# Optimization experiments

Hardware: AMD Instinct MI355X
Metric: run time of the kernel (lower is better)

Reference implementation:

```python
import jax, jax.numpy as jnp
import numpy as np

B, D, U = 64, 256, 256

def setup_inputs() -> dict:
    key = jax.random.key(0)
    ks = jax.random.split(key, 16)
    init_mu = 0.05
    inputs = jax.random.normal(ks[0], (B, D), jnp.float32)
    prev_state = 0.1 * jax.random.normal(ks[1], (B, U), jnp.float32)
    A = jax.random.normal(ks[2], (B, U, U), jnp.float32)
    # symmetric, diagonally boosted covariance-like state
    Sigma_state = 0.01 * (A + jnp.swapaxes(A, 1, 2)) + 0.1 * jnp.eye(U, dtype=jnp.float32)
    def w(k, shape):
        return init_mu * jax.random.normal(k, shape, jnp.float32)
    def s(k):
        return jax.random.uniform(k, (U,), jnp.float32, -4.5, -2.2)
    return {
        'inputs': inputs, 'prev_state': prev_state, 'Sigma_state': Sigma_state,
        'U_z': w(ks[3], (D, U)), 'uz_sigma': s(ks[4]), 'W_z': w(ks[5], (U, U)), 'wz_sigma': s(ks[6]),
        'U_r': w(ks[7], (D, U)), 'ur_sigma': s(ks[8]), 'W_r': w(ks[9], (U, U)), 'wr_sigma': s(ks[10]),
        'U_h': w(ks[11], (D, U)), 'uh_sigma': s(ks[12]), 'W_h': w(ks[13], (U, U)), 'wh_sigma': s(ks[14]),
    }

def _outer(a, b):  # [B,u],[B,u] -> [B,u,u]
    return a[:, :, None] * b[:, None, :]

def _quad(W, S):  # W^T @ S @ W, S is [B,u,u]
    return jnp.matmul(jnp.matmul(W.T, S), W)

def _x_sigma_w(x, sv):  # ||x||^2 * diag(softplus sigma)
    return jnp.sum(x * x, axis=1)[:, None, None] * jnp.diag(sv)

def _tr_sigma_w(S, sv):  # trace(S) * diag(softplus sigma)
    return jnp.trace(S, axis1=1, axis2=2)[:, None, None] * jnp.diag(sv)

def _hadamard_sigma(S1, S2, m1, m2):
    # S1*S2 + diag(m1) S2 diag(m1) + diag(m2) S1 diag(m2) as elementwise/broadcast
    return S1 * S2 + _outer(m1, m1) * S2 + _outer(m2, m2) * S1

def reference(inputs, prev_state, Sigma_state, U_z, uz_sigma, W_z, wz_sigma,
              U_r, ur_sigma, W_r, wr_sigma, U_h, uh_sigma, W_h, wh_sigma):
    sp = jax.nn.softplus
    # --- z gate ---
    az = inputs @ U_z + prev_state @ W_z
    z = jax.nn.sigmoid(az)
    gz = z * (1.0 - z)  # d sigmoid
    Sz = (_quad(W_z, Sigma_state) + _x_sigma_w(prev_state, sp(wz_sigma))
          + _tr_sigma_w(Sigma_state, sp(wz_sigma)) + _x_sigma_w(inputs, sp(uz_sigma)))
    Sigma_out_z = Sz * _outer(gz, gz)
    # --- r gate ---
    ar = inputs @ U_r + prev_state @ W_r
    r = jax.nn.sigmoid(ar)
    gr = r * (1.0 - r)
    Sr = (_quad(W_r, Sigma_state) + _x_sigma_w(prev_state, sp(wr_sigma))
          + _tr_sigma_w(Sigma_state, sp(wr_sigma)) + _x_sigma_w(inputs, sp(ur_sigma)))
    Sigma_out_r = Sr * _outer(gr, gr)
    # --- h candidate ---
    g_in = prev_state * r
    ah = inputs @ U_h + g_in @ W_h
    h = jnp.tanh(ah)
    gh = 1.0 - h * h  # d tanh
    sigma_g = _hadamard_sigma(Sigma_state, Sigma_out_r, prev_state, r)
    Sh = (_quad(W_h, sigma_g) + _x_sigma_w(g_in, sp(wh_sigma))
          + _tr_sigma_w(sigma_g, sp(wh_sigma)) + _x_sigma_w(inputs, sp(uh_sigma)))
    Sigma_out_h = Sh * _outer(gh, gh)
    # --- output combination ---
    mu_out = z * prev_state + (1.0 - z) * h
    sigma_a = _hadamard_sigma(Sigma_out_z, Sigma_state, z, prev_state)
    sigma_b = _hadamard_sigma(Sigma_out_z, Sigma_out_h, 1.0 - z, h)
    Sigma_out = (sigma_a + sigma_b
                 - Sigma_out_z * _outer(prev_state, h)
                 - Sigma_out_z * _outer(h, prev_state))
    Sigma_out = jnp.where(jnp.isnan(Sigma_out) | jnp.isinf(Sigma_out),
                          jnp.zeros_like(Sigma_out), Sigma_out)
    eye = jnp.eye(Sigma_out.shape[-1], dtype=Sigma_out.dtype)
    d = jnp.abs(jnp.diagonal(Sigma_out, axis1=1, axis2=2))
    Sigma_out = Sigma_out * (1.0 - eye) + d[:, :, None] * eye
    return mu_out, Sigma_out
```

## Files before the change

kernel.cpp:

```cpp
#include <hip/hip_runtime.h>
#include <math.h>

#define UDIM 256
#define BATCH 64
#define MATN 65536
#define PITCH 280

typedef __bf16 bf16x8 __attribute__((ext_vector_type(8)));
typedef float  f32x4  __attribute__((ext_vector_type(4)));

__device__ __forceinline__ float softplusf(float x) { return log1pf(expf(x)); }
__device__ __forceinline__ float sigmoidf_(float x) { return 1.f/(1.f+expf(-x)); }

__device__ __forceinline__ bf16x8 frag_load(const __bf16* base, int rt, int kt, int lane) {
  return *(const bf16x8*)(base + (((size_t)(rt*8 + kt))*64 + lane)*8);
}

__device__ __forceinline__ bf16x8 cvt8(const float* p) {
  const float4 f0 = *(const float4*)p;
  const float4 f1 = *(const float4*)(p + 4);
  bf16x8 v;
  v[0]=(__bf16)f0.x; v[1]=(__bf16)f0.y; v[2]=(__bf16)f0.z; v[3]=(__bf16)f0.w;
  v[4]=(__bf16)f1.x; v[5]=(__bf16)f1.y; v[6]=(__bf16)f1.z; v[7]=(__bf16)f1.w;
  return v;
}

__global__ __launch_bounds__(256) void prep6(
    const float* __restrict__ Uz, const float* __restrict__ Wz,
    const float* __restrict__ Ur, const float* __restrict__ Wr,
    const float* __restrict__ Uh, const float* __restrict__ Wh,
    __bf16* __restrict__ Fu_z, __bf16* __restrict__ Fw_z,
    __bf16* __restrict__ Fu_r, __bf16* __restrict__ Fw_r,
    __bf16* __restrict__ Fu_h, __bf16* __restrict__ Fw_h,
    const float* __restrict__ S, const float* __restrict__ x,
    const float* __restrict__ prev, float* __restrict__ scal)
{
  const int t = threadIdx.x;
  if (blockIdx.z == 6) {
    const int blk = blockIdx.y*4 + blockIdx.x;
    const int b = blk*4 + (t >> 6), l = t & 63;
    const float4 xv = *(const float4*)(x + b*UDIM + l*4);
    float s0 = xv.x*xv.x + xv.y*xv.y + xv.z*xv.z + xv.w*xv.w;
    const float4 pv = *(const float4*)(prev + b*UDIM + l*4);
    float s1 = pv.x*pv.x + pv.y*pv.y + pv.z*pv.z + pv.w*pv.w;
    float s2 = 0.f;
#pragma unroll
    for (int e = 0; e < 4; ++e)
      s2 += S[(size_t)b*MATN + (size_t)(l*4 + e)*257];
    for (int off = 32; off; off >>= 1) {
      s0 += __shfl_down(s0, off);
      s1 += __shfl_down(s1, off);
      s2 += __shfl_down(s2, off);
    }
    if (l == 0) {
      atomicAdd(&scal[b], s0);
      atomicAdd(&scal[64 + b], s1);
      atomicAdd(&scal[128 + b], s2);
    }
    return;
  }
  const float* W; __bf16* F;
  switch (blockIdx.z) {
    case 0: W = Uz; F = Fu_z; break;  case 1: W = Wz; F = Fw_z; break;
    case 2: W = Ur; F = Fu_r; break;  case 3: W = Wr; F = Fw_r; break;
    case 4: W = Uh; F = Fu_h; break;  default: W = Wh; F = Fw_h; break;
  }
  const int k0 = blockIdx.y*64, n0 = blockIdx.x*64;
  __shared__ float tile[64][65];
  const int tx = t & 15, ty = t >> 4;
#pragma unroll
  for (int rr = 0; rr < 4; ++rr) {
    const int row = ty*4 + rr;
    const float4 f = *(const float4*)(W + (size_t)(k0 + row)*UDIM + n0 + tx*4);
    tile[row][tx*4+0] = f.x; tile[row][tx*4+1] = f.y;
    tile[row][tx*4+2] = f.z; tile[row][tx*4+3] = f.w;
  }
  __syncthreads();
#pragma unroll
  for (int ss = 0; ss < 2; ++ss) {
    const int s = t + ss*256;
    const int rt_l = s >> 7, kt_l = (s >> 6) & 1, lane = s & 63;
    const int nl = rt_l*16 + (lane & 15), kb = kt_l*32 + (lane >> 4)*8;
    __align__(16) __bf16 tmp[8];
#pragma unroll
    for (int e = 0; e < 8; ++e) tmp[e] = (__bf16)tile[kb + e][nl];
    *(uint4*)(F + (((size_t)((((n0 >> 4) + rt_l)*8) + (k0 >> 5) + kt_l))*64 + lane)*8)
        = *(const uint4*)tmp;
  }
}

__global__ __launch_bounds__(256) void gates_zr(
    const float* __restrict__ x, const float* __restrict__ prev,
    const __bf16* __restrict__ Fu_z, const __bf16* __restrict__ Fw_z,
    const __bf16* __restrict__ Fu_r, const __bf16* __restrict__ Fw_r,
    float* __restrict__ zb, float* __restrict__ rb,
    float* __restrict__ gzb, float* __restrict__ grb,
    float* __restrict__ gin, float* __restrict__ scal)
{
  const int jt = blockIdx.x;
  const int gate = blockIdx.y;
  const __bf16* FU = gate ? Fu_r : Fu_z;
  const __bf16* FW = gate ? Fw_r : Fw_z;
  const int t = threadIdx.x, w = t >> 6, l = t & 63, r = l & 15, q = l >> 4;
  const int mrow = w*16 + r;

  f32x4 acc[4] = {};
#pragma unroll
  for (int ks = 0; ks < 16; ++ks) {
    const int k0 = ks*32;
    const float* asrc; const __bf16* B; int kk;
    if (k0 < 256) { asrc = x    + (size_t)mrow*UDIM + k0         + q*8; B = FU; kk = k0; }
    else          { asrc = prev + (size_t)mrow*UDIM + (k0 - 256) + q*8; B = FW; kk = k0 - 256; }
    const bf16x8 af = cvt8(asrc);
#pragma unroll
    for (int ni = 0; ni < 4; ++ni) {
      const bf16x8 bv = frag_load(B, jt*4 + ni, kk >> 5, l);
      acc[ni] = __builtin_amdgcn_mfma_f32_16x16x32_bf16(af, bv, acc[ni], 0, 0, 0);
    }
  }

  if (gate == 0) {
#pragma unroll
    for (int ni = 0; ni < 4; ++ni) {
      const int n = jt*64 + ni*16 + r;
#pragma unroll
      for (int v = 0; v < 4; ++v) {
        const int m = w*16 + q*4 + v;
        const float zv = sigmoidf_(acc[ni][v]);
        zb[m*UDIM + n]  = zv;
        gzb[m*UDIM + n] = zv * (1.f - zv);
      }
    }
  } else {
    float ggp[4] = {0.f, 0.f, 0.f, 0.f};
#pragma unroll
    for (int ni = 0; ni < 4; ++ni) {
      const int n = jt*64 + ni*16 + r;
#pragma unroll
      for (int v = 0; v < 4; ++v) {
        const int m = w*16 + q*4 + v;
        const float rv = sigmoidf_(acc[ni][v]);
        const float pv = prev[m*UDIM + n];
        const float g2 = pv * rv;
        rb[m*UDIM + n]  = rv;
        grb[m*UDIM + n] = rv * (1.f - rv);
        gin[m*UDIM + n] = g2;
        ggp[v] += g2 * g2;
      }
    }
#pragma unroll
    for (int s = 1; s < 16; s <<= 1)
#pragma unroll
      for (int v = 0; v < 4; ++v) ggp[v] += __shfl_xor(ggp[v], s);
    if (r == 0)
#pragma unroll
      for (int v = 0; v < 4; ++v)
        atomicAdd(&scal[192 + w*16 + q*4 + v], ggp[v]);
  }
}

__global__ __launch_bounds__(256) void gates_h(
    const float* __restrict__ x, const float* __restrict__ gin,
    const __bf16* __restrict__ Fu_h, const __bf16* __restrict__ Fw_h,
    const float* __restrict__ prev, const float* __restrict__ zb,
    float* __restrict__ hb, float* __restrict__ ghb, float* __restrict__ mu_out)
{
  const int jt = blockIdx.x;
  const int t = threadIdx.x, w = t >> 6, l = t & 63, r = l & 15, q = l >> 4;
  const int mrow = w*16 + r;

  f32x4 acc[4] = {};
#pragma unroll
  for (int ks = 0; ks < 16; ++ks) {
    const int k0 = ks*32;
    const float* asrc; const __bf16* B; int kk;
    if (k0 < 256) { asrc = x   + (size_t)mrow*UDIM + k0         + q*8; B = Fu_h; kk = k0; }
    else          { asrc = gin + (size_t)mrow*UDIM + (k0 - 256) + q*8; B = Fw_h; kk = k0 - 256; }
    const bf16x8 af = cvt8(asrc);
#pragma unroll
    for (int ni = 0; ni < 4; ++ni) {
      const bf16x8 bv = frag_load(B, jt*4 + ni, kk >> 5, l);
      acc[ni] = __builtin_amdgcn_mfma_f32_16x16x32_bf16(af, bv, acc[ni], 0, 0, 0);
    }
  }
#pragma unroll
  for (int ni = 0; ni < 4; ++ni) {
    const int n = jt*64 + ni*16 + r;
#pragma unroll
    for (int v = 0; v < 4; ++v) {
      const int m = w*16 + q*4 + v;
      const float hv = tanhf(acc[ni][v]);
      const float zv = zb[m*UDIM + n];
      hb[m*UDIM + n]  = hv;
      ghb[m*UDIM + n] = 1.f - hv*hv;
      mu_out[m*UDIM + n] = zv * prev[m*UDIM + n] + (1.f - zv) * hv;
    }
  }
}

__global__ __launch_bounds__(256, 2) void quad_zr(
    const float* __restrict__ S, const float* __restrict__ prev,
    const float* __restrict__ rb, const float* __restrict__ gzb,
    const float* __restrict__ grb,
    const float* __restrict__ wz_s, const float* __restrict__ uz_s,
    const float* __restrict__ wr_s, const float* __restrict__ ur_s,
    const __bf16* __restrict__ Fw_z, const __bf16* __restrict__ Fw_r,
    float* __restrict__ scal, __bf16* __restrict__ Szb, __bf16* __restrict__ G)
{
  const int bid = blockIdx.x;
  const int s = bid >> 6, b = bid & 63;
  const size_t sb = (size_t)b * MATN;
  const int t = threadIdx.x, w = t >> 6, l = t & 63, r = l & 15, q = l >> 4;

  __shared__ __align__(16) __bf16 Tz[32*PITCH];
  __shared__ __align__(16) __bf16 Tr[32*PITCH];

  f32x4 az[2][4] = {}, ar[2][4] = {};
#pragma unroll
  for (int kt = 0; kt < 8; ++kt) {
    bf16x8 afz[2], afr[2];
#pragma unroll
    for (int mt = 0; mt < 2; ++mt) {
      afz[mt] = frag_load(Fw_z, s*2 + mt, kt, l);
      afr[mt] = frag_load(Fw_r, s*2 + mt, kt, l);
    }
#pragma unroll
    for (int ct = 0; ct < 4; ++ct) {
      const bf16x8 bv = cvt8(S + sb + (size_t)((w*4 + ct)*16 + r)*UDIM + kt*32 + q*8);
#pragma unroll
      for (int mt = 0; mt < 2; ++mt) {
        az[mt][ct] = __builtin_amdgcn_mfma_f32_16x16x32_bf16(afz[mt], bv, az[mt][ct], 0, 0, 0);
        ar[mt][ct] = __builtin_amdgcn_mfma_f32_16x16x32_bf16(afr[mt], bv, ar[mt][ct], 0, 0, 0);
      }
    }
  }
#pragma unroll
  for (int mt = 0; mt < 2; ++mt)
#pragma unroll
    for (int ct = 0; ct < 4; ++ct)
#pragma unroll
      for (int v = 0; v < 4; ++v) {
        const int row = mt*16 + q*4 + v, col = w*64 + ct*16 + r;
        Tz[row*PITCH + col] = (__bf16)az[mt][ct][v];
        Tr[row*PITCH + col] = (__bf16)ar[mt][ct][v];
      }
  __syncthreads();

  f32x4 qz[2][4] = {}, qr[2][4] = {};
#pragma unroll
  for (int kt = 0; kt < 8; ++kt) {
    bf16x8 atz[2], atr[2];
#pragma unroll
    for (int mt = 0; mt < 2; ++mt) {
      atz[mt] = *(const bf16x8*)&Tz[(mt*16 + r)*PITCH + kt*32 + q*8];
      atr[mt] = *(const bf16x8*)&Tr[(mt*16 + r)*PITCH + kt*32 + q*8];
    }
#pragma unroll
    for (int ct = 0; ct < 4; ++ct) {
      const bf16x8 bz = frag_load(Fw_z, w*4 + ct, kt, l);
      const bf16x8 br = frag_load(Fw_r, w*4 + ct, kt, l);
#pragma unroll
      for (int mt = 0; mt < 2; ++mt) {
        qz[mt][ct] = __builtin_amdgcn_mfma_f32_16x16x32_bf16(atz[mt], bz, qz[mt][ct], 0, 0, 0);
        qr[mt][ct] = __builtin_amdgcn_mfma_f32_16x16x32_bf16(atr[mt], br, qr[mt][ct], 0, 0, 0);
      }
    }
  }

  const float xx = scal[b];
  const float dscal = scal[64 + b] + scal[128 + b];

  __align__(16) __bf16 o32[32];
#pragma unroll
  for (int mt = 0; mt < 2; ++mt) {
    const int ib = s*32 + mt*16 + q*4;
    const f32x4 g4 = *(const f32x4*)(gzb + b*UDIM + ib);
#pragma unroll
    for (int ct = 0; ct < 4; ++ct) {
      const int j = (w*4 + ct)*16 + r;
      const float gj = gzb[b*UDIM + j];
#pragma unroll
      for (int v = 0; v < 4; ++v) {
        const int i = ib + v;
        float qv = qz[mt][ct][v];
        if (i == j) qv += dscal*softplusf(wz_s[i]) + xx*softplusf(uz_s[i]);
        o32[mt*16 + ct*4 + v] = (__bf16)(qv * g4[v] * gj);
      }
    }
  }
  {
    __bf16* dst = Szb + ((size_t)(b*8 + s)*256 + t)*32;
#pragma unroll
    for (int e = 0; e < 4; ++e) *(uint4*)(dst + e*8) = *(const uint4*)&o32[e*8];
  }

  float gvals[32];
  float trg = 0.f;
#pragma unroll
  for (int mt = 0; mt < 2; ++mt) {
    const int ib = s*32 + mt*16 + q*4;
    const f32x4 g4 = *(const f32x4*)(grb + b*UDIM + ib);
    const f32x4 p4 = *(const f32x4*)(prev + b*UDIM + ib);
    const f32x4 r4 = *(const f32x4*)(rb + b*UDIM + ib);
#pragma unroll
    for (int ct = 0; ct < 4; ++ct) {
      const int j = (w*4 + ct)*16 + r;
      const float gj = grb[b*UDIM + j];
      const float pj = prev[b*UDIM + j];
      const float rj = rb[b*UDIM + j];
#pragma unroll
      for (int v = 0; v < 4; ++v) {
        const int i = ib + v;
        float qv = qr[mt][ct][v];
        if (i == j) qv += dscal*softplusf(wr_s[i]) + xx*softplusf(ur_s[i]);
        const float Sg = qv * g4[v] * gj;
        const float sv = S[sb + (size_t)i*UDIM + j];
        const float go = Sg*(sv + p4[v]*pj) + r4[v]*rj*sv;
        gvals[mt*16 + ct*4 + v] = go;
        if (i == j) trg += go;
      }
    }
  }
  if (trg != 0.f) atomicAdd(&scal[256 + b], trg);

  __syncthreads();
#pragma unroll
  for (int mt = 0; mt < 2; ++mt)
#pragma unroll
    for (int ct = 0; ct < 4; ++ct)
#pragma unroll
      for (int v = 0; v < 4; ++v)
        Tz[(mt*16 + q*4 + v)*PITCH + w*64 + ct*16 + r] = (__bf16)gvals[mt*16 + ct*4 + v];
  __syncthreads();
#pragma unroll
  for (int ee = 0; ee < 4; ++ee) {
    const int e = ee*256 + t;
    const int chunk = e >> 6, le = e & 63;
    const int rtl = chunk >> 3, kt = chunk & 7;
    const uint4 vv = *(const uint4*)&Tz[(rtl*16 + (le & 15))*PITCH + kt*32 + (le >> 4)*8];
    *(uint4*)(G + sb + (((size_t)((s*2 + rtl)*8 + kt))*64 + le)*8) = vv;
  }
}

__global__ __launch_bounds__(256, 2) void quad_h(
    const float* __restrict__ S, const __bf16* __restrict__ Szb,
    const float* __restrict__ prev, const float* __restrict__ zb,
    const float* __restrict__ hb, const float* __restrict__ ghb,
    const float* __restrict__ wh_s, const float* __restrict__ uh_s,
    const __bf16* __restrict__ Fw_h, const __bf16* __restrict__ G,
    const float* __restrict__ scal, float* __restrict__ out_sig)
{
  const int bid = blockIdx.x;
  const int s = bid >> 6, b = bid & 63;
  const size_t sb = (size_t)b * MATN;
  const int t = threadIdx.x, w = t >> 6, l = t & 63, r = l & 15, q = l >> 4;
  const __bf16* Gb = G + sb;

  __shared__ __align__(16) __bf16 Th[32*PITCH];

  f32x4 ah[2][4] = {};
#pragma unroll
  for (int kt = 0; kt < 8; ++kt) {
    bf16x8 af[2];
#pragma unroll
    for (int mt = 0; mt < 2; ++mt) af[mt] = frag_load(Fw_h, s*2 + mt, kt, l);
#pragma unroll
    for (int ct = 0; ct < 4; ++ct) {
      const bf16x8 bv = frag_load(Gb, w*4 + ct, kt, l);
#pragma unroll
      for (int mt = 0; mt < 2; ++mt)
        ah[mt][ct] = __builtin_amdgcn_mfma_f32_16x16x32_bf16(af[mt], bv, ah[mt][ct], 0, 0, 0);
    }
  }
#pragma unroll
  for (int mt = 0; mt < 2; ++mt)
#pragma unroll
    for (int ct = 0; ct < 4; ++ct)
#pragma unroll
      for (int v = 0; v < 4; ++v)
        Th[(mt*16 + q*4 + v)*PITCH + w*64 + ct*16 + r] = (__bf16)ah[mt][ct][v];
  __syncthreads();

  f32x4 qh[2][4] = {};
#pragma unroll
  for (int kt = 0; kt < 8; ++kt) {
    bf16x8 at[2];
#pragma unroll
    for (int mt = 0; mt < 2; ++mt)
      at[mt] = *(const bf16x8*)&Th[(mt*16 + r)*PITCH + kt*32 + q*8];
#pragma unroll
    for (int ct = 0; ct < 4; ++ct) {
      const bf16x8 bv = frag_load(Fw_h, w*4 + ct, kt, l);
#pragma unroll
      for (int mt = 0; mt < 2; ++mt)
        qh[mt][ct] = __builtin_amdgcn_mfma_f32_16x16x32_bf16(at[mt], bv, qh[mt][ct], 0, 0, 0);
    }
  }

  const float xx = scal[b];
  const float dscal = scal[192 + b] + scal[256 + b];

  const __bf16* szp = Szb + ((size_t)(b*8 + s)*256 + t)*32;
  __align__(16) __bf16 sz32[32];
#pragma unroll
  for (int e = 0; e < 4; ++e) *(uint4*)&sz32[e*8] = *(const uint4*)(szp + e*8);

#pragma unroll
  for (int mt = 0; mt < 2; ++mt) {
    const int ib = s*32 + mt*16 + q*4;
    const f32x4 g4 = *(const f32x4*)(ghb + b*UDIM + ib);
    const f32x4 p4 = *(const f32x4*)(prev + b*UDIM + ib);
    const f32x4 z4 = *(const f32x4*)(zb + b*UDIM + ib);
    const f32x4 h4 = *(const f32x4*)(hb + b*UDIM + ib);
#pragma unroll
    for (int ct = 0; ct < 4; ++ct) {
      const int j = (w*4 + ct)*16 + r;
      const float gj = ghb[b*UDIM + j];
      const float pj = prev[b*UDIM + j];
      const float zj = zb[b*UDIM + j];
      const float hj = hb[b*UDIM + j];
#pragma unroll
      for (int v = 0; v < 4; ++v) {
        const int i = ib + v;
        float qv = qh[mt][ct][v];
        if (i == j) qv += dscal*softplusf(wh_s[i]) + xx*softplusf(uh_s[i]);
        const float Sg = qv * g4[v] * gj;
        const float sv = S[sb + (size_t)i*UDIM + j];
        const float sz = (float)sz32[mt*16 + ct*4 + v];
        float val = sv*(sz + z4[v]*zj)
                  + sz*(p4[v] - h4[v])*(pj - hj)
                  + Sg*(sz + (1.f - z4[v])*(1.f - zj));
        if (!isfinite(val)) val = 0.f;
        if (i == j) val = fabsf(val);
        out_sig[sb + (size_t)i*UDIM + j] = val;
      }
    }
  }
}

extern "C" void kernel_launch(void* const* d_in, const int* in_sizes, int n_in,
                              void* d_out, int out_size, void* d_ws, size_t ws_size,
                              hipStream_t stream) {
  const float* x    = (const float*)d_in[0];
  const float* prev = (const float*)d_in[1];
  const float* S    = (const float*)d_in[2];
  const float* Uz   = (const float*)d_in[3];
  const float* uz_s = (const float*)d_in[4];
  const float* Wz   = (const float*)d_in[5];
  const float* wz_s = (const float*)d_in[6];
  const float* Ur   = (const float*)d_in[7];
  const float* ur_s = (const float*)d_in[8];
  const float* Wr   = (const float*)d_in[9];
  const float* wr_s = (const float*)d_in[10];
  const float* Uh   = (const float*)d_in[11];
  const float* uh_s = (const float*)d_in[12];
  const float* Wh   = (const float*)d_in[13];
  const float* wh_s = (const float*)d_in[14];

  float* out_mu  = (float*)d_out;
  float* out_sig = out_mu + BATCH*UDIM;

  float* ws   = (float*)d_ws;
  float* zb   = ws;
  float* rb   = zb  + BATCH*UDIM;
  float* gzb  = rb  + BATCH*UDIM;
  float* grb  = gzb + BATCH*UDIM;
  float* gin  = grb + BATCH*UDIM;
  float* hb   = gin + BATCH*UDIM;
  float* ghb  = hb  + BATCH*UDIM;
  float* scal = ghb + BATCH*UDIM;
  __bf16* bws  = (__bf16*)(scal + 512);
  __bf16* Fu_z = bws;
  __bf16* Fw_z = Fu_z + MATN;
  __bf16* Fu_r = Fw_z + MATN;
  __bf16* Fw_r = Fu_r + MATN;
  __bf16* Fu_h = Fw_r + MATN;
  __bf16* Fw_h = Fu_h + MATN;
  const size_t BIG = (size_t)BATCH * MATN;
  __bf16* Szb = Fw_h + MATN;
  __bf16* G   = Szb + BIG;

  hipMemsetAsync(scal, 0, 512*sizeof(float), stream);

  prep6<<<dim3(4,4,7), 256, 0, stream>>>(Uz, Wz, Ur, Wr, Uh, Wh,
      Fu_z, Fw_z, Fu_r, Fw_r, Fu_h, Fw_h, S, x, prev, scal);
  gates_zr<<<dim3(4,2), 256, 0, stream>>>(x, prev, Fu_z, Fw_z, Fu_r, Fw_r,
      zb, rb, gzb, grb, gin, scal);
  gates_h<<<dim3(4), 256, 0, stream>>>(x, gin, Fu_h, Fw_h, prev, zb,
      hb, ghb, out_mu);
  quad_zr<<<dim3(512), 256, 0, stream>>>(S, prev, rb, gzb, grb,
      wz_s, uz_s, wr_s, ur_s, Fw_z, Fw_r, scal, Szb, G);
  quad_h<<<dim3(512), 256, 0, stream>>>(S, Szb, prev, zb, hb, ghb,
      wh_s, uh_s, Fw_h, G, scal, out_sig);
}
```

Measured before the change: 179.4 us.

## Pre-convert Sigma to bf16 fragments and halve quad tile rows

Adds a kernel that converts the fp32 Sigma_state once into a bf16 MFMA-fragment layout. quad_zr can then load ready-made fragments instead of converting fp32 on the fly. The quad_zr and quad_h blocks now each compute 16 output rows instead of 32, doubling the grid to 1024 blocks and raising occupancy via launch_bounds(256,4) with smaller shared tiles. The trade-off is an extra full pass over S (fp32 read plus bf16 write), and each block recomputing the first-stage product W^T·S for only 16 rows, which doubles the total S-fragment reads.

```diff
diff --git a/kernel.cpp b/kernel.cpp
--- a/kernel.cpp
+++ b/kernel.cpp
@@ -86,6 +86,24 @@
     for (int e = 0; e < 8; ++e) tmp[e] = (__bf16)tile[kb + e][nl];
     *(uint4*)(F + (((size_t)((((n0 >> 4) + rt_l)*8) + (k0 >> 5) + kt_l))*64 + lane)*8)
         = *(const uint4*)tmp;
+  }
+}
+
+__global__ __launch_bounds__(256) void sconvf(
+    const float* __restrict__ S, __bf16* __restrict__ Sf)
+{
+  const int bx = blockIdx.x, by = blockIdx.y, b = blockIdx.z;
+  const size_t sb = (size_t)b * MATN;
+  const int t = threadIdx.x;
+#pragma unroll
+  for (int ss = 0; ss < 2; ++ss) {
+    const int s = t + ss*256;
+    const int chunk = s >> 6, lane = s & 63;
+    const int rt_l = chunk >> 1, kt_l = chunk & 1;
+    const int row = by*64 + rt_l*16 + (lane & 15);
+    const int col = bx*64 + kt_l*32 + (lane >> 4)*8;
+    const bf16x8 v = cvt8(S + sb + (size_t)row*UDIM + col);
+    *(bf16x8*)(Sf + sb + (((size_t)((by*4 + rt_l)*8 + bx*2 + kt_l))*64 + lane)*8) = v;
   }
 }
 
@@ -198,8 +216,9 @@
   }
 }
 
-__global__ __launch_bounds__(256, 2) void quad_zr(
-    const float* __restrict__ S, const float* __restrict__ prev,
+__global__ __launch_bounds__(256, 4) void quad_zr(
+    const float* __restrict__ S, const __bf16* __restrict__ Sf,
+    const float* __restrict__ prev,
     const float* __restrict__ rb, const float* __restrict__ gzb,
     const float* __restrict__ grb,
     const float* __restrict__ wz_s, const float* __restrict__ uz_s,
@@ -211,70 +230,54 @@
   const int s = bid >> 6, b = bid & 63;
   const size_t sb = (size_t)b * MATN;
   const int t = threadIdx.x, w = t >> 6, l = t & 63, r = l & 15, q = l >> 4;
-
-  __shared__ __align__(16) __bf16 Tz[32*PITCH];
-  __shared__ __align__(16) __bf16 Tr[32*PITCH];
-
-  f32x4 az[2][4] = {}, ar[2][4] = {};
+  const __bf16* Sfb = Sf + sb;
+
+  __shared__ __align__(16) __bf16 Tz[16*PITCH];
+  __shared__ __align__(16) __bf16 Tr[16*PITCH];
+
+  f32x4 az[4] = {}, ar[4] = {};
 #pragma unroll
   for (int kt = 0; kt < 8; ++kt) {
-    bf16x8 afz[2], afr[2];
-#pragma unroll
-    for (int mt = 0; mt < 2; ++mt) {
-      afz[mt] = frag_load(Fw_z, s*2 + mt, kt, l);
-      afr[mt] = frag_load(Fw_r, s*2 + mt, kt, l);
-    }
-#pragma unroll
-    for (int ct = 0; ct < 4; ++ct) {
-      const bf16x8 bv = cvt8(S + sb + (size_t)((w*4 + ct)*16 + r)*UDIM + kt*32 + q*8);
-#pragma unroll
-      for (int mt = 0; mt < 2; ++mt) {
-        az[mt][ct] = __builtin_amdgcn_mfma_f32_16x16x32_bf16(afz[mt], bv, az[mt][ct], 0, 0, 0);
-        ar[mt][ct] = __builtin_amdgcn_mfma_f32_16x16x32_bf16(afr[mt], bv, ar[mt][ct], 0, 0, 0);
-      }
-    }
-  }
-#pragma unroll
-  for (int mt = 0; mt < 2; ++mt)
-#pragma unroll
-    for (int ct = 0; ct < 4; ++ct)
-#pragma unroll
-      for (int v = 0; v < 4; ++v) {
-        const int row = mt*16 + q*4 + v, col = w*64 + ct*16 + r;
-        Tz[row*PITCH + col] = (__bf16)az[mt][ct][v];
-        Tr[row*PITCH + col] = (__bf16)ar[mt][ct][v];
-      }
+    const bf16x8 afz = frag_load(Fw_z, s, kt, l);
+    const bf16x8 afr = frag_load(Fw_r, s, kt, l);
+#pragma unroll
+    for (int ct = 0; ct < 4; ++ct) {
+      const bf16x8 bv = frag_load(Sfb, w*4 + ct, kt, l);
+      az[ct] = __builtin_amdgcn_mfma_f32_16x16x32_bf16(afz, bv, az[ct], 0, 0, 0);
+      ar[ct] = __builtin_amdgcn_mfma_f32_16x16x32_bf16(afr, bv, ar[ct], 0, 0, 0);
+    }
+  }
+#pragma unroll
+  for (int ct = 0; ct < 4; ++ct)
+#pragma unroll
+    for (int v = 0; v < 4; ++v) {
+      const int row = q*4 + v, col = w*64 + ct*16 + r;
+      Tz[row*PITCH + col] = (__bf16)az[ct][v];
+      Tr[row*PITCH + col] = (__bf16)ar[ct][v];
+    }
   __syncthreads();
 
-  f32x4 qz[2][4] = {}, qr[2][4] = {};
+  f32x4 qz[4] = {}, qr[4] = {};
 #pragma unroll
   for (int kt = 0; kt < 8; ++kt) {
-    bf16x8 atz[2], atr[2];
-#pragma unroll
-    for (int mt = 0; mt < 2; ++mt) {
-      atz[mt] = *(const bf16x8*)&Tz[(mt*16 + r)*PITCH + kt*32 + q*8];
-      atr[mt] = *(const bf16x8*)&Tr[(mt*16 + r)*PITCH + kt*32 + q*8];
-    }
+    const bf16x8 atz = *(const bf16x8*)&Tz[r*PITCH + kt*32 + q*8];
+    const bf16x8 atr = *(const bf16x8*)&Tr[r*PITCH + kt*32 + q*8];
 #pragma unroll
     for (int ct = 0; ct < 4; ++ct) {
       const bf16x8 bz = frag_load(Fw_z, w*4 + ct, kt, l);
       const bf16x8 br = frag_load(Fw_r, w*4 + ct, kt, l);
-#pragma unroll
-      for (int mt = 0; mt < 2; ++mt) {
-        qz[mt][ct] = __builtin_amdgcn_mfma_f32_16x16x32_bf16(atz[mt], bz, qz[mt][ct], 0, 0, 0);
-        qr[mt][ct] = __builtin_amdgcn_mfma_f32_16x16x32_bf16(atr[mt], br, qr[mt][ct], 0, 0, 0);
-      }
+      qz[ct] = __builtin_amdgcn_mfma_f32_16x16x32_bf16(atz, bz, qz[ct], 0, 0, 0);
+      qr[ct] = __builtin_amdgcn_mfma_f32_16x16x32_bf16(atr, br, qr[ct], 0, 0, 0);
     }
   }
 
   const float xx = scal[b];
   const float dscal = scal[64 + b] + scal[128 + b];
-
-  __align__(16) __bf16 o32[32];
-#pragma unroll
-  for (int mt = 0; mt < 2; ++mt) {
-    const int ib = s*32 + mt*16 + q*4;
+  const int ib = s*16 + q*4;
+
+  {
     const f32x4 g4 = *(const f32x4*)(gzb + b*UDIM + ib);
+    __align__(16) __bf16 o16[16];
 #pragma unroll
     for (int ct = 0; ct < 4; ++ct) {
       const int j = (w*4 + ct)*16 + r;
@@ -282,23 +285,19 @@
 #pragma unroll
       for (int v = 0; v < 4; ++v) {
         const int i = ib + v;
-        float qv = qz[mt][ct][v];
+        float qv = qz[ct][v];
         if (i == j) qv += dscal*softplusf(wz_s[i]) + xx*softplusf(uz_s[i]);
-        o32[mt*16 + ct*4 + v] = (__bf16)(qv * g4[v] * gj);
+        o16[ct*4 + v] = (__bf16)(qv * g4[v] * gj);
       }
     }
-  }
+    __bf16* dst = Szb + ((size_t)(b*16 + s)*256 + t)*16;
+    *(uint4*)dst       = *(const uint4*)&o16[0];
+    *(uint4*)(dst + 8) = *(const uint4*)&o16[8];
+  }
+
+  float gvals[16];
+  float trg = 0.f;
   {
-    __bf16* dst = Szb + ((size_t)(b*8 + s)*256 + t)*32;
-#pragma unroll
-    for (int e = 0; e < 4; ++e) *(uint4*)(dst + e*8) = *(const uint4*)&o32[e*8];
-  }
-
-  float gvals[32];
-  float trg = 0.f;
-#pragma unroll
-  for (int mt = 0; mt < 2; ++mt) {
-    const int ib = s*32 + mt*16 + q*4;
     const f32x4 g4 = *(const f32x4*)(grb + b*UDIM + ib);
     const f32x4 p4 = *(const f32x4*)(prev + b*UDIM + ib);
     const f32x4 r4 = *(const f32x4*)(rb + b*UDIM + ib);
@@ -311,12 +310,12 @@
 #pragma unroll
       for (int v = 0; v < 4; ++v) {
         const int i = ib + v;
-        float qv = qr[mt][ct][v];
+        float qv = qr[ct][v];
         if (i == j) qv += dscal*softplusf(wr_s[i]) + xx*softplusf(ur_s[i]);
         const float Sg = qv * g4[v] * gj;
         const float sv = S[sb + (size_t)i*UDIM + j];
         const float go = Sg*(sv + p4[v]*pj) + r4[v]*rj*sv;
-        gvals[mt*16 + ct*4 + v] = go;
+        gvals[ct*4 + v] = go;
         if (i == j) trg += go;
       }
     }
@@ -325,24 +324,21 @@
 
   __syncthreads();
 #pragma unroll
-  for (int mt = 0; mt < 2; ++mt)
-#pragma unroll
-    for (int ct = 0; ct < 4; ++ct)
-#pragma unroll
-      for (int v = 0; v < 4; ++v)
-        Tz[(mt*16 + q*4 + v)*PITCH + w*64 + ct*16 + r] = (__bf16)gvals[mt*16 + ct*4 + v];
+  for (int ct = 0; ct < 4; ++ct)
+#pragma unroll
+    for (int v = 0; v < 4; ++v)
+      Tz[(q*4 + v)*PITCH + w*64 + ct*16 + r] = (__bf16)gvals[ct*4 + v];
   __syncthreads();
 #pragma unroll
-  for (int ee = 0; ee < 4; ++ee) {
-    const int e = ee*256 + t;
-    const int chunk = e >> 6, le = e & 63;
-    const int rtl = chunk >> 3, kt = chunk & 7;
-    const uint4 vv = *(const uint4*)&Tz[(rtl*16 + (le & 15))*PITCH + kt*32 + (le >> 4)*8];
-    *(uint4*)(G + sb + (((size_t)((s*2 + rtl)*8 + kt))*64 + le)*8) = vv;
-  }
-}
-
-__global__ __launch_bounds__(256, 2) void quad_h(
+  for (int ee = 0; ee < 2; ++ee) {
+    const int e = t + ee*256;
+    const int kt = e >> 6, le = e & 63;
+    const uint4 vv = *(const uint4*)&Tz[(le & 15)*PITCH + kt*32 + (le >> 4)*8];
+    *(uint4*)(G + sb + (((size_t)(s*8 + kt))*64 + le)*8) = vv;
+  }
+}
+
+__global__ __launch_bounds__(256, 4) void quad_h(
     const float* __restrict__ S, const __bf16* __restrict__ Szb,
     const float* __restrict__ prev, const float* __restrict__ zb,
     const float* __restrict__ hb, const float* __restrict__ ghb,
@@ -356,84 +352,71 @@
   const int t = threadIdx.x, w = t >> 6, l = t & 63, r = l & 15, q = l >> 4;
   const __bf16* Gb = G + sb;
 
-  __shared__ __align__(16) __bf16 Th[32*PITCH];
-
-  f32x4 ah[2][4] = {};
+  __shared__ __align__(16) __bf16 Th[16*PITCH];
+
+  f32x4 ah[4] = {};
 #pragma unroll
   for (int kt = 0; kt < 8; ++kt) {
-    bf16x8 af[2];
-#pragma unroll
-    for (int mt = 0; mt < 2; ++mt) af[mt] = frag_load(Fw_h, s*2 + mt, kt, l);
+    const bf16x8 af = frag_load(Fw_h, s, kt, l);
 #pragma unroll
     for (int ct = 0; ct < 4; ++ct) {
       const bf16x8 bv = frag_load(Gb, w*4 + ct, kt, l);
-#pragma unroll
-      for (int mt = 0; mt < 2; ++mt)
-        ah[mt][ct] = __builtin_amdgcn_mfma_f32_16x16x32_bf16(af[mt], bv, ah[mt][ct], 0, 0, 0);
-    }
-  }
-#pragma unroll
-  for (int mt = 0; mt < 2; ++mt)
-#pragma unroll
-    for (int ct = 0; ct < 4; ++ct)
-#pragma unroll
-      for (int v = 0; v < 4; ++v)
-        Th[(mt*16 + q*4 + v)*PITCH + w*64 + ct*16 + r] = (__bf16)ah[mt][ct][v];
+      ah[ct] = __builtin_amdgcn_mfma_f32_16x16x32_bf16(af, bv, ah[ct], 0, 0, 0);
+    }
+  }
+#pragma unroll
+  for (int ct = 0; ct < 4; ++ct)
+#pragma unroll
+    for (int v = 0; v < 4; ++v)
+      Th[(q*4 + v)*PITCH + w*64 + ct*16 + r] = (__bf16)ah[ct][v];
   __syncthreads();
 
-  f32x4 qh[2][4] = {};
+  f32x4 qh[4] = {};
 #pragma unroll
   for (int kt = 0; kt < 8; ++kt) {
-    bf16x8 at[2];
-#pragma unroll
-    for (int mt = 0; mt < 2; ++mt)
-      at[mt] = *(const bf16x8*)&Th[(mt*16 + r)*PITCH + kt*32 + q*8];
+    const bf16x8 at = *(const bf16x8*)&Th[r*PITCH + kt*32 + q*8];
 #pragma unroll
     for (int ct = 0; ct < 4; ++ct) {
       const bf16x8 bv = frag_load(Fw_h, w*4 + ct, kt, l);
-#pragma unroll
-      for (int mt = 0; mt < 2; ++mt)
-        qh[mt][ct] = __builtin_amdgcn_mfma_f32_16x16x32_bf16(at[mt], bv, qh[mt][ct], 0, 0, 0);
+      qh[ct] = __builtin_amdgcn_mfma_f32_16x16x32_bf16(at, bv, qh[ct], 0, 0, 0);
     }
   }
 
   const float xx = scal[b];
   const float dscal = scal[192 + b] + scal[256 + b];
-
-  const __bf16* szp = Szb + ((size_t)(b*8 + s)*256 + t)*32;
-  __align__(16) __bf16 sz32[32];
-#pragma unroll
-  for (int e = 0; e < 4; ++e) *(uint4*)&sz32[e*8] = *(const uint4*)(szp + e*8);
-
-#pragma unroll
-  for (int mt = 0; mt < 2; ++mt) {
-    const int ib = s*32 + mt*16 + q*4;
-    const f32x4 g4 = *(const f32x4*)(ghb + b*UDIM + ib);
-    const f32x4 p4 = *(const f32x4*)(prev + b*UDIM + ib);
-    const f32x4 z4 = *(const f32x4*)(zb + b*UDIM + ib);
-    const f32x4 h4 = *(const f32x4*)(hb + b*UDIM + ib);
-#pragma unroll
-    for (int ct = 0; ct < 4; ++ct) {
-      const int j = (w*4 + ct)*16 + r;
-      const float gj = ghb[b*UDIM + j];
-      const float pj = prev[b*UDIM + j];
-      const float zj = zb[b*UDIM + j];
-      const float hj = hb[b*UDIM + j];
-#pragma unroll
-      for (int v = 0; v < 4; ++v) {
-        const int i = ib + v;
-        float qv = qh[mt][ct][v];
-        if (i == j) qv += dscal*softplusf(wh_s[i]) + xx*softplusf(uh_s[i]);
-        const float Sg = qv * g4[v] * gj;
-        const float sv = S[sb + (size_t)i*UDIM + j];
-        const float sz = (float)sz32[mt*16 + ct*4 + v];
-        float val = sv*(sz + z4[v]*zj)
-                  + sz*(p4[v] - h4[v])*(pj - hj)
-                  + Sg*(sz + (1.f - z4[v])*(1.f - zj));
-        if (!isfinite(val)) val = 0.f;
-        if (i == j) val = fabsf(val);
-        out_sig[sb + (size_t)i*UDIM + j] = val;
-      }
+  const int ib = s*16 + q*4;
+
+  const __bf16* szp = Szb + ((size_t)(b*16 + s)*256 + t)*16;
+  __align__(16) __bf16 sz16[16];
+  *(uint4*)&sz16[0] = *(const uint4*)szp;
+  *(uint4*)&sz16[8] = *(const uint4*)(szp + 8);
+
+  const f32x4 g4 = *(const f32x4*)(ghb + b*UDIM + ib);
+  const f32x4 p4 = *(const f32x4*)(prev + b*UDIM + ib);
+  const f32x4 z4 = *(const f32x4*)(zb + b*UDIM + ib);
+  const f32x4 h4 = *(const f32x4*)(hb + b*UDIM + ib);
+
+#pragma unroll
+  for (int ct = 0; ct < 4; ++ct) {
+    const int j = (w*4 + ct)*16 + r;
+    const float gj = ghb[b*UDIM + j];
+    const float pj = prev[b*UDIM + j];
+    const float zj = zb[b*UDIM + j];
+    const float hj = hb[b*UDIM + j];
+#pragma unroll
+    for (int v = 0; v < 4; ++v) {
+      const int i = ib + v;
+      float qv = qh[ct][v];
+      if (i == j) qv += dscal*softplusf(wh_s[i]) + xx*softplusf(uh_s[i]);
+      const float Sg = qv * g4[v] * gj;
+      const float sv = S[sb + (size_t)i*UDIM + j];
+      const float sz = (float)sz16[ct*4 + v];
+      float val = sv*(sz + z4[v]*zj)
+                + sz*(p4[v] - h4[v])*(pj - hj)
+                + Sg*(sz + (1.f - z4[v])*(1.f - zj));
+      if (!isfinite(val)) val = 0.f;
+      if (i == j) val = fabsf(val);
+      out_sig[sb + (size_t)i*UDIM + j] = val;
     }
   }
 }
@@ -479,17 +462,19 @@
   const size_t BIG = (size_t)BATCH * MATN;
   __bf16* Szb = Fw_h + MATN;
   __bf16* G   = Szb + BIG;
+  __bf16* Sf  = G + BIG;
 
   hipMemsetAsync(scal, 0, 512*sizeof(float), stream);
 
   prep6<<<dim3(4,4,7), 256, 0, stream>>>(Uz, Wz, Ur, Wr, Uh, Wh,
       Fu_z, Fw_z, Fu_r, Fw_r, Fu_h, Fw_h, S, x, prev, scal);
+  sconvf<<<dim3(4,4,64), 256, 0, stream>>>(S, Sf);
   gates_zr<<<dim3(4,2), 256, 0, stream>>>(x, prev, Fu_z, Fw_z, Fu_r, Fw_r,
       zb, rb, gzb, grb, gin, scal);
   gates_h<<<dim3(4), 256, 0, stream>>>(x, gin, Fu_h, Fw_h, prev, zb,
       hb, ghb, out_mu);
-  quad_zr<<<dim3(512), 256, 0, stream>>>(S, prev, rb, gzb, grb,
+  quad_zr<<<dim3(1024), 256, 0, stream>>>(S, Sf, prev, rb, gzb, grb,
       wz_s, uz_s, wr_s, ur_s, Fw_z, Fw_r, scal, Szb, G);
-  quad_h<<<dim3(512), 256, 0, stream>>>(S, Szb, prev, zb, hb, ghb,
+  quad_h<<<dim3(1024), 256, 0, stream>>>(S, Szb, prev, zb, hb, ghb,
       wh_s, uh_s, Fw_h, G, scal, out_sig);
 }
```

After: 176.6 us. No clear change (-1.5%).
